# Optimization experiments

Measured on AMD Instinct MI355X. Metric: run time of the kernel, lower is better.

Reference implementation:

```python
import jax, jax.numpy as jnp
import numpy as np

S = 14
L_COORD = 5.0
L_NOOBJ = 0.5

def setup_inputs() -> dict:
    key = jax.random.key(0)
    k1, k2, k3, k4 = jax.random.split(key, 4)
    N = 4096
    pred_tensor = jax.random.uniform(k1, (N, S, S, 30), jnp.float32, 0.1, 0.9)
    target_boxes = jax.random.uniform(k2, (N, S, S, 4), jnp.float32, 0.1, 0.9)
    target_cls = jax.random.uniform(k3, (N, S, S, 20), jnp.float32, 0.0, 1.0)
    has_object_map = jax.random.bernoulli(k4, 0.25, (N, S, S))
    return {"pred_tensor": pred_tensor, "target_boxes": target_boxes,
            "target_cls": target_cls, "has_object_map": has_object_map}

def _xywh2xyxy(b):
    # Faithful to the original (including its quirk: x2 = w/S + w/2, not x/S + w/2)
    x, y, w, h = b[..., 0], b[..., 1], b[..., 2], b[..., 3]
    return jnp.stack([x / S - w / 2, y / S - h / 2,
                      w / S + w / 2, h / S + h / 2], axis=-1)

def _pairwise_iou(p, t):
    # p: (..., B, 4) xyxy, t: (..., 4) xyxy -> iou: (..., B)
    # Elementwise per-cell IoU: equals diagonal of the original NxM matrix.
    lt = jnp.maximum(p[..., :2], t[..., None, :2])
    rb = jnp.minimum(p[..., 2:], t[..., None, 2:])
    wh = jnp.clip(rb - lt, 0.0)
    inter = wh[..., 0] * wh[..., 1]
    a1 = (p[..., 2] - p[..., 0]) * (p[..., 3] - p[..., 1])
    a2 = (t[..., 2] - t[..., 0]) * (t[..., 3] - t[..., 1])
    return inter / (a1 + a2[..., None] - inter)

def reference(pred_tensor, target_boxes, target_cls, has_object_map):
    N = pred_tensor.shape[0]
    mask = has_object_map                       # (N,S,S) bool
    pred_boxes = pred_tensor[..., :10].reshape(*pred_tensor.shape[:3], 2, 5)  # (N,S,S,B,5)
    pred_cls = pred_tensor[..., 10:30]

    # classification loss over object cells
    cls_loss = jnp.sum(jnp.where(mask[..., None],
                                 jnp.square(pred_cls - target_cls), 0.0))

    # no-object confidence loss over non-object cells, for both boxes
    conf = pred_boxes[..., 4]                   # (N,S,S,B)
    no_obj_loss = L_NOOBJ * jnp.sum(jnp.where(~mask[..., None],
                                              jnp.square(conf), 0.0))

    # best-of-B selection via per-cell IoU (original extracted NxM diagonal)
    tgt_xyxy = _xywh2xyxy(target_boxes)         # (N,S,S,4)
    pred_xyxy = _xywh2xyxy(pred_boxes[..., :4]) # (N,S,S,B,4)
    ious = _pairwise_iou(pred_xyxy, tgt_xyxy)   # (N,S,S,B)
    best_iou = jnp.max(ious, axis=-1)           # (N,S,S)
    idx = jnp.argmax(ious, axis=-1)             # (N,S,S)
    best_xyxy = jnp.take_along_axis(pred_xyxy, idx[..., None, None], axis=3)[..., 0, :]
    best_conf = jnp.take_along_axis(conf, idx[..., None], axis=3)[..., 0]

    d_xy = jnp.square(tgt_xyxy[..., 0] - best_xyxy[..., 0]) \
         + jnp.square(tgt_xyxy[..., 1] - best_xyxy[..., 1])
    d_wh = jnp.square(jnp.sqrt(tgt_xyxy[..., 2]) - jnp.sqrt(best_xyxy[..., 2])) \
         + jnp.square(jnp.sqrt(tgt_xyxy[..., 3]) - jnp.sqrt(best_xyxy[..., 3]))
    reg_loss = L_COORD * jnp.sum(jnp.where(mask, d_xy + d_wh, 0.0))

    # containing-object confidence loss; best_iou is treated as ground truth
    contain_loss = jnp.sum(jnp.where(
        mask, jnp.square(best_conf - jax.lax.stop_gradient(best_iou)), 0.0))

    total = cls_loss + no_obj_loss + reg_loss + contain_loss
    Nf = jnp.asarray(N, pred_tensor.dtype)
    # [total, reg, containing_obj, no_obj, cls], each averaged over batch
    return jnp.stack([total, reg_loss, contain_loss, no_obj_loss, cls_loss]) / Nf
```

## Files before the change

kernel.cpp:

```cpp
#include <hip/hip_runtime.h>

#define SGRID 14
#define L_COORD 5.0f
#define L_NOOBJ 0.5f
#define NBLOCKS 1024
#define NTHREADS 256
#define RTHREADS 256


__global__ __launch_bounds__(NTHREADS) void yolo_main(const float* __restrict__ pred,
                                                      const float* __restrict__ tbox,
                                                      const float* __restrict__ tcls,
                                                      const void* __restrict__ maskp,
                                                      float4* __restrict__ partial,
                                                      int n_cells) {
    __shared__ int fmt_s;
    if (threadIdx.x == 0) fmt_s = 0;
    __syncthreads();
    {
        const uint4 mv = ((const uint4*)maskp)[threadIdx.x];
        if ((mv.x | mv.y | mv.z | mv.w) > 1u) atomicOr(&fmt_s, 1);
    }
    __syncthreads();
    const bool bytefmt = (fmt_s != 0);

    float reg = 0.f, contain = 0.f, noobj = 0.f, cls = 0.f;
    constexpr float invS = 1.0f / (float)SGRID;
    constexpr float sA = invS + 0.5f;

    for (int cell = blockIdx.x * blockDim.x + threadIdx.x; cell < n_cells;
         cell += NBLOCKS * NTHREADS) {
        bool mask = bytefmt ? (((const unsigned char*)maskp)[cell] != 0)
                            : (((const int*)maskp)[cell] != 0);
        const float* p = pred + (size_t)cell * 30;

        if (mask) {
            float pv[30];
            #pragma unroll
            for (int k = 0; k < 15; ++k) {
                float2 v = ((const float2*)p)[k];
                pv[2 * k] = v.x; pv[2 * k + 1] = v.y;
            }
            float4 tb = ((const float4*)tbox)[cell];
            float tx1 = tb.x * invS - 0.5f * tb.z;
            float ty1 = tb.y * invS - 0.5f * tb.w;
            float tx2 = tb.z * sA;
            float ty2 = tb.w * sA;
            float ta = (tx2 - tx1) * (ty2 - ty1);

            float bx1[2], by1[2], bx2[2], by2[2], conf[2], iou[2];
            #pragma unroll
            for (int b = 0; b < 2; ++b) {
                float x = pv[b * 5 + 0], y = pv[b * 5 + 1];
                float w = pv[b * 5 + 2], h = pv[b * 5 + 3];
                conf[b] = pv[b * 5 + 4];
                bx1[b] = x * invS - 0.5f * w;
                by1[b] = y * invS - 0.5f * h;
                bx2[b] = w * sA;
                by2[b] = h * sA;
                float ltx = fmaxf(bx1[b], tx1), lty = fmaxf(by1[b], ty1);
                float rbx = fminf(bx2[b], tx2), rby = fminf(by2[b], ty2);
                float iw = fmaxf(rbx - ltx, 0.f), ih = fmaxf(rby - lty, 0.f);
                float inter = iw * ih;
                float a1 = (bx2[b] - bx1[b]) * (by2[b] - by1[b]);
                iou[b] = inter / (a1 + ta - inter);
            }
            int idx = (iou[1] > iou[0]) ? 1 : 0;
            float biou = fmaxf(iou[0], iou[1]);

            float dx = tx1 - bx1[idx], dy = ty1 - by1[idx];
            float dxy = dx * dx + dy * dy;
            float sw = sqrtf(tx2) - sqrtf(bx2[idx]);
            float sh = sqrtf(ty2) - sqrtf(by2[idx]);
            float dwh = sw * sw + sh * sh;
            reg += L_COORD * (dxy + dwh);

            float dc = conf[idx] - biou;
            contain += dc * dc;

            const float4* tc = (const float4*)(tcls + (size_t)cell * 20);
            float c = 0.f;
            #pragma unroll
            for (int k = 0; k < 5; ++k) {
                float4 tt = tc[k];
                float d0 = pv[10 + 4 * k + 0] - tt.x;
                float d1 = pv[10 + 4 * k + 1] - tt.y;
                float d2 = pv[10 + 4 * k + 2] - tt.z;
                float d3 = pv[10 + 4 * k + 3] - tt.w;
                c += d0 * d0 + d1 * d1 + d2 * d2 + d3 * d3;
            }
            cls += c;
        } else {
            float c0 = p[4], c1 = p[9];
            noobj += L_NOOBJ * (c0 * c0 + c1 * c1);
        }
    }

    #pragma unroll
    for (int off = 32; off > 0; off >>= 1) {
        reg     += __shfl_down(reg, off, 64);
        contain += __shfl_down(contain, off, 64);
        noobj   += __shfl_down(noobj, off, 64);
        cls     += __shfl_down(cls, off, 64);
    }
    __shared__ float sred[NTHREADS / 64][4];
    int wid = threadIdx.x >> 6, lane = threadIdx.x & 63;
    if (lane == 0) { sred[wid][0] = reg; sred[wid][1] = contain; sred[wid][2] = noobj; sred[wid][3] = cls; }
    __syncthreads();
    if (threadIdx.x == 0) {
        float r = 0.f, c = 0.f, n = 0.f, cl = 0.f;
        #pragma unroll
        for (int w = 0; w < NTHREADS / 64; ++w) { r += sred[w][0]; c += sred[w][1]; n += sred[w][2]; cl += sred[w][3]; }
        partial[blockIdx.x] = make_float4(r, c, n, cl);
    }
}

__global__ __launch_bounds__(RTHREADS) void reduce_final(const float4* __restrict__ partial,
                                                         float* __restrict__ out, float invN) {
    double r = 0.0, c = 0.0, n = 0.0, cl = 0.0;
    #pragma unroll
    for (int k = 0; k < NBLOCKS / RTHREADS; ++k) {
        float4 v = partial[threadIdx.x + k * RTHREADS];
        r += v.x; c += v.y; n += v.z; cl += v.w;
    }
    #pragma unroll
    for (int off = 32; off > 0; off >>= 1) {
        r  += __shfl_down(r, off, 64);
        c  += __shfl_down(c, off, 64);
        n  += __shfl_down(n, off, 64);
        cl += __shfl_down(cl, off, 64);
    }
    __shared__ double sred[4][4];
    int wid = threadIdx.x >> 6, lane = threadIdx.x & 63;
    if (lane == 0) { sred[wid][0] = r; sred[wid][1] = c; sred[wid][2] = n; sred[wid][3] = cl; }
    __syncthreads();
    if (threadIdx.x == 0) {
        double R = 0.0, C = 0.0, Nn = 0.0, Cl = 0.0;
        #pragma unroll
        for (int w = 0; w < 4; ++w) { R += sred[w][0]; C += sred[w][1]; Nn += sred[w][2]; Cl += sred[w][3]; }
        double total = R + C + Nn + Cl;
        out[0] = (float)(total * (double)invN);
        out[1] = (float)(R * (double)invN);
        out[2] = (float)(C * (double)invN);
        out[3] = (float)(Nn * (double)invN);
        out[4] = (float)(Cl * (double)invN);
    }
}

extern "C" void kernel_launch(void* const* d_in, const int* in_sizes, int n_in,
                              void* d_out, int out_size, void* d_ws, size_t ws_size,
                              hipStream_t stream) {
    const float* pred = (const float*)d_in[0];
    const float* tbox = (const float*)d_in[1];
    const float* tcls = (const float*)d_in[2];
    const void*  mask = d_in[3];
    int n_cells = in_sizes[3];
    int N = n_cells / (SGRID * SGRID);

    float4* partial = (float4*)d_ws;

    yolo_main<<<NBLOCKS, NTHREADS, 0, stream>>>(pred, tbox, tcls, mask, partial, n_cells);
    reduce_final<<<1, RTHREADS, 0, stream>>>(partial, (float*)d_out, 1.0f / (float)N);
}
```

Baseline: 30.89 us.

## Process two cells per thread with float4 loads and one-shot grid

Each thread now handles an adjacent pair of cells, so the 60-float prediction block is 16-byte aligned and can be loaded with float4 vectors instead of float2. The mask is read as a packed pair. The grid-stride loop over a fixed 1024 blocks becomes a single pass with one thread per pair, about 1568 blocks, and the final reduce takes a variable partial count. The aim is fewer, wider memory transactions and more memory-level parallelism. The cost is higher register pressure from two 30-float arrays and more partials to reduce.

```diff
diff --git a/kernel.cpp b/kernel.cpp
--- a/kernel.cpp
+++ b/kernel.cpp
@@ -3,17 +3,71 @@
 #define SGRID 14
 #define L_COORD 5.0f
 #define L_NOOBJ 0.5f
-#define NBLOCKS 1024
 #define NTHREADS 256
 #define RTHREADS 256
 
+
+__device__ __forceinline__ void cell_loss(const float (&pv)[30], float4 tb,
+                                          const float4* __restrict__ tc,
+                                          float& reg, float& contain, float& cls) {
+    constexpr float invS = 1.0f / (float)SGRID;
+    constexpr float sA = invS + 0.5f;
+
+    float tx1 = tb.x * invS - 0.5f * tb.z;
+    float ty1 = tb.y * invS - 0.5f * tb.w;
+    float tx2 = tb.z * sA;
+    float ty2 = tb.w * sA;
+    float ta = (tx2 - tx1) * (ty2 - ty1);
+
+    float bx1[2], by1[2], bx2[2], by2[2], conf[2], iou[2];
+    #pragma unroll
+    for (int b = 0; b < 2; ++b) {
+        float x = pv[b * 5 + 0], y = pv[b * 5 + 1];
+        float w = pv[b * 5 + 2], h = pv[b * 5 + 3];
+        conf[b] = pv[b * 5 + 4];
+        bx1[b] = x * invS - 0.5f * w;
+        by1[b] = y * invS - 0.5f * h;
+        bx2[b] = w * sA;
+        by2[b] = h * sA;
+        float ltx = fmaxf(bx1[b], tx1), lty = fmaxf(by1[b], ty1);
+        float rbx = fminf(bx2[b], tx2), rby = fminf(by2[b], ty2);
+        float iw = fmaxf(rbx - ltx, 0.f), ih = fmaxf(rby - lty, 0.f);
+        float inter = iw * ih;
+        float a1 = (bx2[b] - bx1[b]) * (by2[b] - by1[b]);
+        iou[b] = inter / (a1 + ta - inter);
+    }
+    int idx = (iou[1] > iou[0]) ? 1 : 0;
+    float biou = fmaxf(iou[0], iou[1]);
+
+    float dx = tx1 - bx1[idx], dy = ty1 - by1[idx];
+    float dxy = dx * dx + dy * dy;
+    float sw = sqrtf(tx2) - sqrtf(bx2[idx]);
+    float sh = sqrtf(ty2) - sqrtf(by2[idx]);
+    float dwh = sw * sw + sh * sh;
+    reg += L_COORD * (dxy + dwh);
+
+    float dc = conf[idx] - biou;
+    contain += dc * dc;
+
+    float c = 0.f;
+    #pragma unroll
+    for (int k = 0; k < 5; ++k) {
+        float4 tt = tc[k];
+        float d0 = pv[10 + 4 * k + 0] - tt.x;
+        float d1 = pv[10 + 4 * k + 1] - tt.y;
+        float d2 = pv[10 + 4 * k + 2] - tt.z;
+        float d3 = pv[10 + 4 * k + 3] - tt.w;
+        c += d0 * d0 + d1 * d1 + d2 * d2 + d3 * d3;
+    }
+    cls += c;
+}
 
 __global__ __launch_bounds__(NTHREADS) void yolo_main(const float* __restrict__ pred,
                                                       const float* __restrict__ tbox,
                                                       const float* __restrict__ tcls,
                                                       const void* __restrict__ maskp,
                                                       float4* __restrict__ partial,
-                                                      int n_cells) {
+                                                      int npairs) {
     __shared__ int fmt_s;
     if (threadIdx.x == 0) fmt_s = 0;
     __syncthreads();
@@ -25,73 +79,54 @@
     const bool bytefmt = (fmt_s != 0);
 
     float reg = 0.f, contain = 0.f, noobj = 0.f, cls = 0.f;
-    constexpr float invS = 1.0f / (float)SGRID;
-    constexpr float sA = invS + 0.5f;
-
-    for (int cell = blockIdx.x * blockDim.x + threadIdx.x; cell < n_cells;
-         cell += NBLOCKS * NTHREADS) {
-        bool mask = bytefmt ? (((const unsigned char*)maskp)[cell] != 0)
-                            : (((const int*)maskp)[cell] != 0);
-        const float* p = pred + (size_t)cell * 30;
-
-        if (mask) {
-            float pv[30];
+
+    const int pair = blockIdx.x * NTHREADS + threadIdx.x;
+    if (pair < npairs) {
+        bool m0, m1;
+        if (bytefmt) {
+            unsigned short mm = ((const unsigned short*)maskp)[pair];
+            m0 = (mm & 0xFFu) != 0; m1 = (mm >> 8) != 0;
+        } else {
+            int2 mm = ((const int2*)maskp)[pair];
+            m0 = mm.x != 0; m1 = mm.y != 0;
+        }
+
+        const float* p = pred + (size_t)pair * 60;
+        float pv0[30], pv1[30];
+
+        if (m0) {
             #pragma unroll
-            for (int k = 0; k < 15; ++k) {
-                float2 v = ((const float2*)p)[k];
-                pv[2 * k] = v.x; pv[2 * k + 1] = v.y;
+            for (int k = 0; k < 7; ++k) {
+                float4 v = ((const float4*)p)[k];
+                pv0[4 * k + 0] = v.x; pv0[4 * k + 1] = v.y;
+                pv0[4 * k + 2] = v.z; pv0[4 * k + 3] = v.w;
             }
-            float4 tb = ((const float4*)tbox)[cell];
-            float tx1 = tb.x * invS - 0.5f * tb.z;
-            float ty1 = tb.y * invS - 0.5f * tb.w;
-            float tx2 = tb.z * sA;
-            float ty2 = tb.w * sA;
-            float ta = (tx2 - tx1) * (ty2 - ty1);
-
-            float bx1[2], by1[2], bx2[2], by2[2], conf[2], iou[2];
+            float2 t = ((const float2*)p)[14];
+            pv0[28] = t.x; pv0[29] = t.y;
+        }
+        if (m1) {
+            float2 t = ((const float2*)p)[15];
+            pv1[0] = t.x; pv1[1] = t.y;
             #pragma unroll
-            for (int b = 0; b < 2; ++b) {
-                float x = pv[b * 5 + 0], y = pv[b * 5 + 1];
-                float w = pv[b * 5 + 2], h = pv[b * 5 + 3];
-                conf[b] = pv[b * 5 + 4];
-                bx1[b] = x * invS - 0.5f * w;
-                by1[b] = y * invS - 0.5f * h;
-                bx2[b] = w * sA;
-                by2[b] = h * sA;
-                float ltx = fmaxf(bx1[b], tx1), lty = fmaxf(by1[b], ty1);
-                float rbx = fminf(bx2[b], tx2), rby = fminf(by2[b], ty2);
-                float iw = fmaxf(rbx - ltx, 0.f), ih = fmaxf(rby - lty, 0.f);
-                float inter = iw * ih;
-                float a1 = (bx2[b] - bx1[b]) * (by2[b] - by1[b]);
-                iou[b] = inter / (a1 + ta - inter);
+            for (int k = 0; k < 7; ++k) {
+                float4 v = ((const float4*)(p + 32))[k];
+                pv1[2 + 4 * k + 0] = v.x; pv1[2 + 4 * k + 1] = v.y;
+                pv1[2 + 4 * k + 2] = v.z; pv1[2 + 4 * k + 3] = v.w;
             }
-            int idx = (iou[1] > iou[0]) ? 1 : 0;
-            float biou = fmaxf(iou[0], iou[1]);
-
-            float dx = tx1 - bx1[idx], dy = ty1 - by1[idx];
-            float dxy = dx * dx + dy * dy;
-            float sw = sqrtf(tx2) - sqrtf(bx2[idx]);
-            float sh = sqrtf(ty2) - sqrtf(by2[idx]);
-            float dwh = sw * sw + sh * sh;
-            reg += L_COORD * (dxy + dwh);
-
-            float dc = conf[idx] - biou;
-            contain += dc * dc;
-
-            const float4* tc = (const float4*)(tcls + (size_t)cell * 20);
-            float c = 0.f;
-            #pragma unroll
-            for (int k = 0; k < 5; ++k) {
-                float4 tt = tc[k];
-                float d0 = pv[10 + 4 * k + 0] - tt.x;
-                float d1 = pv[10 + 4 * k + 1] - tt.y;
-                float d2 = pv[10 + 4 * k + 2] - tt.z;
-                float d3 = pv[10 + 4 * k + 3] - tt.w;
-                c += d0 * d0 + d1 * d1 + d2 * d2 + d3 * d3;
-            }
-            cls += c;
-        } else {
+        }
+        float4 tb0 = make_float4(0.f, 0.f, 0.f, 0.f);
+        float4 tb1 = make_float4(0.f, 0.f, 0.f, 0.f);
+        if (m0) tb0 = ((const float4*)tbox)[2 * pair];
+        if (m1) tb1 = ((const float4*)tbox)[2 * pair + 1];
+
+        if (m0) cell_loss(pv0, tb0, (const float4*)(tcls + (size_t)(2 * pair) * 20), reg, contain, cls);
+        else {
             float c0 = p[4], c1 = p[9];
+            noobj += L_NOOBJ * (c0 * c0 + c1 * c1);
+        }
+        if (m1) cell_loss(pv1, tb1, (const float4*)(tcls + (size_t)(2 * pair + 1) * 20), reg, contain, cls);
+        else {
+            float c0 = p[34], c1 = p[39];
             noobj += L_NOOBJ * (c0 * c0 + c1 * c1);
         }
     }
@@ -116,11 +151,11 @@
 }
 
 __global__ __launch_bounds__(RTHREADS) void reduce_final(const float4* __restrict__ partial,
+                                                         int nparts,
                                                          float* __restrict__ out, float invN) {
     double r = 0.0, c = 0.0, n = 0.0, cl = 0.0;
-    #pragma unroll
-    for (int k = 0; k < NBLOCKS / RTHREADS; ++k) {
-        float4 v = partial[threadIdx.x + k * RTHREADS];
+    for (int k = threadIdx.x; k < nparts; k += RTHREADS) {
+        float4 v = partial[k];
         r += v.x; c += v.y; n += v.z; cl += v.w;
     }
     #pragma unroll
@@ -156,9 +191,11 @@
     const void*  mask = d_in[3];
     int n_cells = in_sizes[3];
     int N = n_cells / (SGRID * SGRID);
+    int npairs = n_cells / 2;
 
     float4* partial = (float4*)d_ws;
 
-    yolo_main<<<NBLOCKS, NTHREADS, 0, stream>>>(pred, tbox, tcls, mask, partial, n_cells);
-    reduce_final<<<1, RTHREADS, 0, stream>>>(partial, (float*)d_out, 1.0f / (float)N);
-}
+    int blocks = (npairs + NTHREADS - 1) / NTHREADS;
+    yolo_main<<<blocks, NTHREADS, 0, stream>>>(pred, tbox, tcls, mask, partial, npairs);
+    reduce_final<<<1, RTHREADS, 0, stream>>>(partial, blocks, (float*)d_out, 1.0f / (float)N);
+}
```

After: 32.68 us. +5.8%, slower.
